# Performance work log

Measured on AMD Instinct MI355X. Metric: run time of the kernel, lower is better.

## Reference

```python
import jax, jax.numpy as jnp
import numpy as np


def setup_inputs() -> dict:
    key = jax.random.key(0)
    k1, k2, k3, k4, k5 = jax.random.split(key, 5)
    B, H, W, C = 4, 64, 64, 256
    d = C // 8
    return {
        "x": jax.random.normal(k1, (B, H, W, C), dtype=jnp.float32),
        "Wf": jax.random.normal(k2, (C, d), dtype=jnp.float32) * 0.05,
        "Wg": jax.random.normal(k3, (C, d), dtype=jnp.float32) * 0.05,
        "Wh": jax.random.normal(k4, (C, C), dtype=jnp.float32) * 0.05,
        "gamma": jax.random.normal(k5, (1,), dtype=jnp.float32),
    }


def reference(x, Wf, Wg, Wh, gamma):
    # x: [B,H,W,C]; 1x1 convs (no bias) == channel matmuls
    B, H, W, C = x.shape
    N = H * W
    f = jnp.einsum('bhwc,cd->bhwd', x, Wf).reshape(B, N, -1)  # keys  [B,N,d]
    g = jnp.einsum('bhwc,cd->bhwd', x, Wg).reshape(B, N, -1)  # query [B,N,d]
    h = jnp.einsum('bhwc,ce->bhwe', x, Wh).reshape(B, N, -1)  # value [B,N,C]
    s = jnp.einsum('bnd,bmd->bnm', g, f)       # [B,N,N], no 1/sqrt(d) scale (faithful)
    beta = jax.nn.softmax(s, axis=-1)
    o = jnp.einsum('bnm,bmc->bnc', beta, h).reshape(B, H, W, C)
    return gamma * o + x
```

## Files before the change

### kernel.cpp

```cpp
#include <hip/hip_runtime.h>
#include <math.h>

#define B_   4
#define N_   4096
#define C_   256
#define D_   32
#define QT   64
#define KTB  128
#define NT2  (N_/KTB)
#define L2E  1.4426950408889634f

typedef __attribute__((ext_vector_type(8)))  short  short8;
typedef __attribute__((ext_vector_type(4)))  float  f32x4;
typedef __attribute__((ext_vector_type(16))) float  f32x16;

__device__ __forceinline__ unsigned short f2bf(float f) {
    unsigned int u = __builtin_bit_cast(unsigned int, f);
    u += 0x7fffu + ((u >> 16) & 1u);
    return (unsigned short)(u >> 16);
}
__device__ __forceinline__ unsigned pack2(float lo, float hi) {
    return (unsigned)f2bf(lo) | ((unsigned)f2bf(hi) << 16);
}
__device__ __forceinline__ unsigned pack2rn(float lo, float hi) {
    unsigned ul = __builtin_bit_cast(unsigned, lo) + 0x8000u;
    unsigned uh = __builtin_bit_cast(unsigned, hi) + 0x8000u;
    return (ul >> 16) | (uh & 0xffff0000u);
}

__global__ __launch_bounds__(64) void wcast(const float* __restrict__ Wf,
        const float* __restrict__ Wg, const float* __restrict__ Wh,
        unsigned short* __restrict__ WT) {
    const int e = blockIdx.x;
    const int t = threadIdx.x;
    const float* src; int stride, col;
    if (e < 256)      { src = Wh; stride = 256; col = e; }
    else if (e < 288) { src = Wf; stride = 32;  col = e - 256; }
    else              { src = Wg; stride = 32;  col = e - 288; }
    const int c0 = t * 4;
    __align__(8) unsigned short tmp[4];
    #pragma unroll
    for (int i = 0; i < 4; ++i)
        tmp[i] = f2bf(src[(size_t)(c0 + i) * stride + col]);
    *(uint2*)(WT + (size_t)e * 256 + c0) = *(const uint2*)tmp;
}

__global__ __launch_bounds__(256, 2) void proj(const float* __restrict__ x,
        const unsigned short* __restrict__ WT,
        unsigned short* __restrict__ f, unsigned short* __restrict__ g,
        unsigned short* __restrict__ hT) {
    __shared__ unsigned short xb[32 * 256];
    const int t = threadIdx.x;
    const int l = t & 63, w = t >> 6;
    const long n0 = (long)blockIdx.x * 32;
    const int b = (int)(n0 >> 12), nloc = (int)(n0 & 4095);

    {
        const int r = t >> 3, ch = (t & 7) * 32;
        const float* xp = x + (n0 + r) * C_ + ch;
        #pragma unroll
        for (int m4 = 0; m4 < 8; ++m4) {
            float4 v = *(const float4*)(xp + m4 * 4);
            unsigned u0 = pack2(v.x, v.y), u1 = pack2(v.z, v.w);
            const int byte = (r * 512 + (ch + m4 * 4) * 2) ^ ((r & 7) << 4);
            *(uint2*)((char*)xb + byte) = make_uint2(u0, u1);
        }
    }
    __syncthreads();

    const int l15 = l & 15, l31 = l & 31;
    const int l4 = (l >> 4) & 3, hi = (l >> 5) & 1;

    f32x16 acc0, acc1;
    #pragma unroll
    for (int i = 0; i < 16; ++i) { acc0[i] = 0.f; acc1[i] = 0.f; }
    const int e0 = w * 64 + l31;
    #pragma unroll
    for (int ks = 0; ks < 16; ++ks) {
        short8 A = *(const short8*)((const char*)xb +
                    ((l31 * 512 + ks * 32 + hi * 16) ^ ((l31 & 7) << 4)));
        short8 B0 = *(const short8*)(WT + (size_t)e0 * 256 + ks * 16 + hi * 8);
        short8 B1 = *(const short8*)(WT + (size_t)(e0 + 32) * 256 + ks * 16 + hi * 8);
        acc0 = __builtin_amdgcn_mfma_f32_32x32x16_bf16(A, B0, acc0, 0, 0, 0);
        acc1 = __builtin_amdgcn_mfma_f32_32x32x16_bf16(A, B1, acc1, 0, 0, 0);
    }
    f32x4 fgacc[2];
    #pragma unroll
    for (int rf = 0; rf < 2; ++rf)
        #pragma unroll
        for (int i = 0; i < 4; ++i) fgacc[rf][i] = 0.f;
    const int fcol = w * 16 + l15;
    #pragma unroll
    for (int ks2 = 0; ks2 < 8; ++ks2) {
        short8 Bf = *(const short8*)(WT + (size_t)(256 + fcol) * 256 + ks2 * 32 + l4 * 8);
        #pragma unroll
        for (int rf = 0; rf < 2; ++rf) {
            const int row = rf * 16 + l15;
            short8 A = *(const short8*)((const char*)xb +
                        ((row * 512 + ks2 * 64 + l4 * 16) ^ ((row & 7) << 4)));
            fgacc[rf] = __builtin_amdgcn_mfma_f32_16x16x32_bf16(A, Bf, fgacc[rf], 0, 0, 0);
        }
    }

    #pragma unroll
    for (int ef = 0; ef < 2; ++ef) {
        const f32x16& a = ef ? acc1 : acc0;
        const int e = e0 + ef * 32;
        unsigned short* dp = hT + ((size_t)b * C_ + e) * N_ + nloc + 4 * hi;
        #pragma unroll
        for (int qd = 0; qd < 4; ++qd) {
            unsigned u0 = pack2(a[4*qd+0], a[4*qd+1]);
            unsigned u1 = pack2(a[4*qd+2], a[4*qd+3]);
            *(uint2*)(dp + 8 * qd) = make_uint2(u0, u1);
        }
    }
    {
        unsigned short* outp = (fcol < 32) ? (f + fcol) : (g + fcol - 32);
        #pragma unroll
        for (int rf = 0; rf < 2; ++rf)
            #pragma unroll
            for (int r = 0; r < 4; ++r) {
                const int row = rf * 16 + l4 * 4 + r;
                outp[(size_t)(n0 + row) * D_] = f2bf(fgacc[rf][r]);
            }
    }
}

__global__ __launch_bounds__(512, 2) void attn(
        const unsigned short* __restrict__ g,
        const unsigned short* __restrict__ f,
        const unsigned short* __restrict__ hT,
        const float* __restrict__ x,
        const float* __restrict__ gammap,
        float* __restrict__ out) {

    __shared__ unsigned short P[2][QT * KTB];
    __shared__ float Lpart[8][4][16];
    __shared__ float linv[QT];

    const int t = threadIdx.x, l = t & 63, w = t >> 6;
    const int b = blockIdx.y, q0 = blockIdx.x * QT;
    const long nb = (long)b * N_;
    const unsigned short* hb = hT + (size_t)b * C_ * N_;

    {
        uint4* pz = (uint4*)&P[0][0];
        pz[t] = make_uint4(0,0,0,0);       pz[t+512]  = make_uint4(0,0,0,0);
        pz[t+1024] = make_uint4(0,0,0,0);  pz[t+1536] = make_uint4(0,0,0,0);
    }

    const int l15 = l & 15, l31 = l & 31;
    const int l4 = (l >> 4) & 3, hi = (l >> 5) & 1;

    short8 gB[4];
    #pragma unroll
    for (int qf = 0; qf < 4; ++qf)
        gB[qf] = *(const short8*)(g + (size_t)(nb + q0 + qf*16 + l15) * D_ + l4*8);

    const int ecol = w * 32 + l31;
    const unsigned short* hcol = hb + (size_t)ecol * N_ + hi * 8;
    const size_t fbase = (size_t)(nb + w*16 + l15) * D_ + l4*8;

    const int pwB = ((w*2 + (l4>>1))*64 + l15)*16 + (l4&1)*8;
    const int prB = hi*1024 + l31*16;

    float la[4] = {0.f, 0.f, 0.f, 0.f};
    f32x16 acc0, acc1;
    #pragma unroll
    for (int i = 0; i < 16; ++i) { acc0[i] = 0.f; acc1[i] = 0.f; }

    short8 fA[2], hB[2][8];
    fA[0] = *(const short8*)(f + fbase);
    fA[1] = *(const short8*)(f + fbase + (size_t)KTB * D_);
    #pragma unroll
    for (int kk = 0; kk < 8; ++kk) {
        hB[0][kk] = *(const short8*)(hcol + kk * 16);
        hB[1][kk] = *(const short8*)(hcol + (size_t)KTB + kk * 16);
    }

    f32x4 S[4];

#define QK(slot) { \
    f32x4 zz; zz[0]=0.f; zz[1]=0.f; zz[2]=0.f; zz[3]=0.f; \
    _Pragma("unroll") \
    for (int qf = 0; qf < 4; ++qf) \
        S[qf] = __builtin_amdgcn_mfma_f32_16x16x32_bf16(fA[slot], gB[qf], zz, 0,0,0); \
}

#define EXPAND(buf) { \
    _Pragma("unroll") \
    for (int qf = 0; qf < 4; ++qf) { \
        float p0 = exp2f(fminf(S[qf][0],60.f)*L2E); \
        float p1 = exp2f(fminf(S[qf][1],60.f)*L2E); \
        float p2 = exp2f(fminf(S[qf][2],60.f)*L2E); \
        float p3 = exp2f(fminf(S[qf][3],60.f)*L2E); \
        la[qf] += (p0+p1)+(p2+p3); \
        *(uint2*)((char*)&P[buf][0] + pwB + qf*256) = \
            make_uint2(pack2rn(p0,p1), pack2rn(p2,p3)); \
    } \
}

#define BODY(CUR, NXT, kvar, DO_N, DO_PF) { \
    __syncthreads(); \
    if (DO_N) QK(NXT); \
    _Pragma("unroll") \
    for (int kk = 0; kk < 8; ++kk) { \
        short8 a0 = *(const short8*)((const char*)&P[CUR][0] + kk*2048 + prB); \
        short8 a1 = *(const short8*)((const char*)&P[CUR][0] + kk*2048 + prB + 512); \
        acc0 = __builtin_amdgcn_mfma_f32_32x32x16_bf16(a0, hB[CUR][kk], acc0, 0,0,0); \
        acc1 = __builtin_amdgcn_mfma_f32_32x32x16_bf16(a1, hB[CUR][kk], acc1, 0,0,0); \
    } \
    if (DO_PF) { \
        const int ktp = ((kvar) + 2) & (NT2 - 1); \
        fA[CUR] = *(const short8*)(f + fbase + (size_t)ktp * KTB * D_); \
        _Pragma("unroll") \
        for (int kk = 0; kk < 8; ++kk) \
            hB[CUR][kk] = *(const short8*)(hcol + (size_t)ktp * KTB + kk * 16); \
    } \
    if (DO_N) EXPAND(NXT); \
}

    QK(0);
    __syncthreads();
    EXPAND(0);

    #pragma unroll 1
    for (int k = 0; k < NT2 - 2; k += 2) {
        BODY(0, 1, k,     true, true);
        BODY(1, 0, k + 1, true, true);
    }
    BODY(0, 1, NT2 - 2, true,  false);
    BODY(1, 0, NT2 - 1, false, false);
#undef BODY
#undef EXPAND
#undef QK

    #pragma unroll
    for (int qf = 0; qf < 4; ++qf) {
        la[qf] += __shfl_xor(la[qf], 16, 64);
        la[qf] += __shfl_xor(la[qf], 32, 64);
    }
    if (l < 16) {
        #pragma unroll
        for (int qf = 0; qf < 4; ++qf) Lpart[w][qf][l] = la[qf];
    }
    __syncthreads();
    if (t < QT) {
        const int qf = t >> 4, r = t & 15;
        float s = 0.f;
        #pragma unroll
        for (int ww = 0; ww < 8; ++ww) s += Lpart[ww][qf][r];
        linv[t] = 1.f / fmaxf(s, 1e-30f);
    }
    __syncthreads();

    const float gamma = gammap[0];
    #pragma unroll
    for (int qh = 0; qh < 2; ++qh) {
        const f32x16& a = qh ? acc1 : acc0;
        #pragma unroll
        for (int reg = 0; reg < 16; ++reg) {
            const int row = qh*32 + (reg & 3) + 8*(reg >> 2) + 4*hi;
            const size_t o = (size_t)(nb + q0 + row) * C_ + ecol;
            out[o] = fmaf(gamma, a[reg] * linv[row], x[o]);
        }
    }
}

extern "C" void kernel_launch(void* const* d_in, const int* in_sizes, int n_in,
                              void* d_out, int out_size, void* d_ws, size_t ws_size,
                              hipStream_t stream) {
    const float* x     = (const float*)d_in[0];
    const float* Wf    = (const float*)d_in[1];
    const float* Wg    = (const float*)d_in[2];
    const float* Wh    = (const float*)d_in[3];
    const float* gamma = (const float*)d_in[4];
    float* out = (float*)d_out;

    unsigned short* WT  = (unsigned short*)d_ws;
    unsigned short* fb  = WT + 320 * 256;
    unsigned short* gb  = fb + (size_t)B_ * N_ * D_;
    unsigned short* hTb = gb + (size_t)B_ * N_ * D_;

    wcast<<<dim3(320), dim3(64), 0, stream>>>(Wf, Wg, Wh, WT);
    proj <<<dim3(B_ * N_ / 32), dim3(256), 0, stream>>>(x, WT, fb, gb, hTb);
    attn <<<dim3(N_ / QT, B_), dim3(512), 0, stream>>>(gb, fb, hTb, x, gamma, out);
}
```

Measured before the change: 99.71 us.

## Split attention keys across two blocks and combine partial results in a new kernel

The attention kernel now splits the key dimension in half (split-K), so the grid grows from 256 to 512 blocks. Each block writes unnormalized partial outputs and partial row sums. A new combine kernel adds the two halves, normalizes them, and applies the gamma residual. The block index is also remapped so that adjacent block IDs cover different query tiles, batches and halves. The aim is better CU occupancy on the GPU, at the cost of roughly 32MB of extra partial-output traffic and one more launch. The split relies on there being no max subtraction, since exp is clamped instead, which is why the partial sums can simply be added.

Result: slower. 109.7 us (+10.1%).

```diff
diff --git a/kernel.cpp b/kernel.cpp
--- a/kernel.cpp
+++ b/kernel.cpp
@@ -7,7 +7,7 @@
 #define D_   32
 #define QT   64
 #define KTB  128
-#define NT2  (N_/KTB)
+#define TPH  16
 #define L2E  1.4426950408889634f
 
 typedef __attribute__((ext_vector_type(8)))  short  short8;
@@ -130,17 +130,20 @@
         const unsigned short* __restrict__ g,
         const unsigned short* __restrict__ f,
         const unsigned short* __restrict__ hT,
-        const float* __restrict__ x,
-        const float* __restrict__ gammap,
-        float* __restrict__ out) {
+        float* __restrict__ pO0, float* __restrict__ pO1,
+        float* __restrict__ lp) {
 
     __shared__ unsigned short P[2][QT * KTB];
     __shared__ float Lpart[8][4][16];
-    __shared__ float linv[QT];
+
+    const int s = ((int)blockIdx.x & 7) * 64 + ((int)blockIdx.x >> 3);
+    const int q0 = (s & 63) * QT;
+    const int b  = (s >> 6) & 3;
+    const int z  = (s >> 8) & 1;
 
     const int t = threadIdx.x, l = t & 63, w = t >> 6;
-    const int b = blockIdx.y, q0 = blockIdx.x * QT;
     const long nb = (long)b * N_;
+    const size_t khalf = (size_t)z * (N_ / 2);
     const unsigned short* hb = hT + (size_t)b * C_ * N_;
 
     {
@@ -158,8 +161,8 @@
         gB[qf] = *(const short8*)(g + (size_t)(nb + q0 + qf*16 + l15) * D_ + l4*8);
 
     const int ecol = w * 32 + l31;
-    const unsigned short* hcol = hb + (size_t)ecol * N_ + hi * 8;
-    const size_t fbase = (size_t)(nb + w*16 + l15) * D_ + l4*8;
+    const unsigned short* hcol = hb + (size_t)ecol * N_ + khalf + hi * 8;
+    const size_t fbase = (size_t)(nb + w*16 + l15) * D_ + khalf * D_ + l4*8;
 
     const int pwB = ((w*2 + (l4>>1))*64 + l15)*16 + (l4&1)*8;
     const int prB = hi*1024 + l31*16;
@@ -211,7 +214,7 @@
         acc1 = __builtin_amdgcn_mfma_f32_32x32x16_bf16(a1, hB[CUR][kk], acc1, 0,0,0); \
     } \
     if (DO_PF) { \
-        const int ktp = ((kvar) + 2) & (NT2 - 1); \
+        const int ktp = ((kvar) + 2) & (TPH - 1); \
         fA[CUR] = *(const short8*)(f + fbase + (size_t)ktp * KTB * D_); \
         _Pragma("unroll") \
         for (int kk = 0; kk < 8; ++kk) \
@@ -225,12 +228,12 @@
     EXPAND(0);
 
     #pragma unroll 1
-    for (int k = 0; k < NT2 - 2; k += 2) {
+    for (int k = 0; k < TPH - 2; k += 2) {
         BODY(0, 1, k,     true, true);
         BODY(1, 0, k + 1, true, true);
     }
-    BODY(0, 1, NT2 - 2, true,  false);
-    BODY(1, 0, NT2 - 1, false, false);
+    BODY(0, 1, TPH - 2, true,  false);
+    BODY(1, 0, TPH - 1, false, false);
 #undef BODY
 #undef EXPAND
 #undef QK
@@ -247,24 +250,40 @@
     __syncthreads();
     if (t < QT) {
         const int qf = t >> 4, r = t & 15;
-        float s = 0.f;
-        #pragma unroll
-        for (int ww = 0; ww < 8; ++ww) s += Lpart[ww][qf][r];
-        linv[t] = 1.f / fmaxf(s, 1e-30f);
-    }
-    __syncthreads();
-
-    const float gamma = gammap[0];
+        float sm = 0.f;
+        #pragma unroll
+        for (int ww = 0; ww < 8; ++ww) sm += Lpart[ww][qf][r];
+        lp[(size_t)z * (B_ * N_) + nb + q0 + t] = sm;
+    }
+
+    float* pout = z ? pO1 : pO0;
     #pragma unroll
     for (int qh = 0; qh < 2; ++qh) {
         const f32x16& a = qh ? acc1 : acc0;
         #pragma unroll
         for (int reg = 0; reg < 16; ++reg) {
             const int row = qh*32 + (reg & 3) + 8*(reg >> 2) + 4*hi;
-            const size_t o = (size_t)(nb + q0 + row) * C_ + ecol;
-            out[o] = fmaf(gamma, a[reg] * linv[row], x[o]);
+            pout[(size_t)(nb + q0 + row) * C_ + ecol] = a[reg];
         }
     }
+}
+
+__global__ __launch_bounds__(256) void combine(const float* __restrict__ pO1,
+        const float* __restrict__ lp, const float* __restrict__ x,
+        const float* __restrict__ gammap, float* __restrict__ outp) {
+    const size_t i4 = (size_t)blockIdx.x * 256 + threadIdx.x;
+    const size_t row = i4 >> 6;
+    const float linv = 1.f / fmaxf(lp[row] + lp[(size_t)(B_*N_) + row], 1e-30f);
+    const float gm = gammap[0];
+    float4 a  = ((const float4*)outp)[i4];
+    float4 bq = ((const float4*)pO1)[i4];
+    float4 xv = ((const float4*)x)[i4];
+    float4 r;
+    r.x = fmaf(gm, (a.x + bq.x) * linv, xv.x);
+    r.y = fmaf(gm, (a.y + bq.y) * linv, xv.y);
+    r.z = fmaf(gm, (a.z + bq.z) * linv, xv.z);
+    r.w = fmaf(gm, (a.w + bq.w) * linv, xv.w);
+    ((float4*)outp)[i4] = r;
 }
 
 extern "C" void kernel_launch(void* const* d_in, const int* in_sizes, int n_in,
@@ -281,8 +300,12 @@
     unsigned short* fb  = WT + 320 * 256;
     unsigned short* gb  = fb + (size_t)B_ * N_ * D_;
     unsigned short* hTb = gb + (size_t)B_ * N_ * D_;
-
-    wcast<<<dim3(320), dim3(64), 0, stream>>>(Wf, Wg, Wh, WT);
-    proj <<<dim3(B_ * N_ / 32), dim3(256), 0, stream>>>(x, WT, fb, gb, hTb);
-    attn <<<dim3(N_ / QT, B_), dim3(512), 0, stream>>>(gb, fb, hTb, x, gamma, out);
-}
+    float* pO1 = (float*)(hTb + (size_t)B_ * C_ * N_);
+    float* lpb = pO1 + (size_t)B_ * N_ * C_;
+
+    wcast  <<<dim3(320), dim3(64), 0, stream>>>(Wf, Wg, Wh, WT);
+    proj   <<<dim3(B_ * N_ / 32), dim3(256), 0, stream>>>(x, WT, fb, gb, hTb);
+    attn   <<<dim3(512), dim3(512), 0, stream>>>(gb, fb, hTb, out, pO1, lpb);
+    combine<<<dim3(B_ * N_ * C_ / 4 / 256), dim3(256), 0, stream>>>(
+            pO1, lpb, x, gamma, out);
+}
```
